# Kernel optimization log

Hardware: AMD Instinct MI355X
Metric: run time of the kernel (lower is better)

## Reference

```python
import jax, jax.numpy as jnp
import numpy as np
from jax import lax

LAYER_NUM = 6
EPS = 1e-9
BN_EPS = 1e-5

# CNOT ring on 3 qubits: CNOT(0,1), CNOT(1,2), CNOT(2,0); qubit 0 = MSB.
_P = np.zeros((8, 8), np.float32)
for _b in range(8):
    b0, b1, b2 = (_b >> 2) & 1, (_b >> 1) & 1, _b & 1
    b1 ^= b0
    b2 ^= b1
    b0 ^= b2
    _P[(b0 << 2) | (b1 << 1) | b2, _b] = 1.0
CNOT_RING = jnp.asarray(_P)


def _ry(t):
    c, s = jnp.cos(t / 2), jnp.sin(t / 2)
    return jnp.stack([jnp.stack([c, -s]), jnp.stack([s, c])])


def _channel_unitary(wc):
    # wc: [layer_num, 3] rotation angles -> full 8x8 circuit unitary (real, RY+CNOT)
    U = jnp.eye(8, dtype=wc.dtype)
    for l in range(wc.shape[0]):
        K = jnp.kron(jnp.kron(_ry(wc[l, 0]), _ry(wc[l, 1])), _ry(wc[l, 2]))
        U = CNOT_RING @ K @ U
    return U


def qcnn(x, weights, out_dim, out_size):
    # x: [B, C, H, W]; weights: [C, layer_num, 3]; 2x2 kernel, stride 2, no padding
    B, C, H, W = x.shape
    OH, OW = H // 2, W // 2
    # im2col: [B, C*4, OH, OW] with feature dim ordered (C, kh, kw)
    patches = lax.conv_general_dilated_patches(x, (2, 2), (2, 2), 'VALID')
    patches = patches.reshape(B, C, 4, OH * OW).transpose(0, 1, 3, 2)  # [B,C,P,4]
    # amplitude embedding on 2 data qubits, ancilla (MSB) in |0>
    nrm = jnp.linalg.norm(patches, axis=-1, keepdims=True)
    amp = patches / jnp.maximum(nrm, EPS)
    psi0 = jnp.pad(amp, ((0, 0), (0, 0), (0, 0), (0, 4)))  # [B,C,P,8]
    U = jax.vmap(_channel_unitary)(weights)  # [C,8,8]
    psi = jnp.einsum('cjk,bcpk->bcpj', U, psi0)
    probs = psi * psi
    data = probs[..., :4]  # post-select ancilla = 0
    data = data / jnp.maximum(data.sum(-1, keepdims=True), EPS)
    return data.reshape(B, out_dim, out_size, out_size)


def batchnorm2d(x, gamma, beta):
    mean = x.mean(axis=(0, 2, 3), keepdims=True)
    var = x.var(axis=(0, 2, 3), keepdims=True)
    xn = (x - mean) * lax.rsqrt(var + BN_EPS)
    return xn * gamma[None, :, None, None] + beta[None, :, None, None]


def setup_inputs() -> dict:
    key = jax.random.key(0)
    ks = jax.random.split(key, 5)
    return {
        'z': jax.random.normal(ks[0], (1024, 256, 4, 4), jnp.float32),
        'w1': jax.random.normal(ks[1], (256, LAYER_NUM, 3), jnp.float32),
        'w2': jax.random.normal(ks[2], (64, LAYER_NUM, 3), jnp.float32),
        'w3': jax.random.normal(ks[3], (16, LAYER_NUM, 3), jnp.float32),
        'w4': jax.random.normal(ks[4], (4, LAYER_NUM, 3), jnp.float32),
        'gamma2': jnp.ones((64,), jnp.float32), 'beta2': jnp.zeros((64,), jnp.float32),
        'gamma3': jnp.ones((16,), jnp.float32), 'beta3': jnp.zeros((16,), jnp.float32),
        'gamma4': jnp.ones((4,), jnp.float32), 'beta4': jnp.zeros((4,), jnp.float32),
        'gamma_f': jnp.ones((1,), jnp.float32), 'beta_f': jnp.zeros((1,), jnp.float32),
    }


def reference(z, w1, w2, w3, w4, gamma2, beta2, gamma3, beta3, gamma4, beta4, gamma_f, beta_f):
    s1 = qcnn(z, w1, 64, 8)
    x = jax.nn.relu(batchnorm2d(s1, gamma2, beta2))
    s2 = qcnn(x, w2, 16, 16)
    x = jax.nn.relu(batchnorm2d(s2, gamma3, beta3))
    s3 = qcnn(x, w3, 4, 32)
    x = jax.nn.relu(batchnorm2d(s3, gamma4, beta4))
    s4 = qcnn(x, w4, 1, 64)
    s4_bn = batchnorm2d(s4, gamma_f, beta_f)
    return jnp.tanh(s4_bn), s4, s4_bn
```

## Files before the change

kernel.cpp:

```cpp
#include <hip/hip_runtime.h>
#include <math.h>


#define NB 1024

__global__ __launch_bounds__(256) void build_V_kernel(
    const float* __restrict__ w1, const float* __restrict__ w2,
    const float* __restrict__ w3, const float* __restrict__ w4,
    float* __restrict__ V, float* __restrict__ acc)
{
    int t = blockIdx.x * blockDim.x + threadIdx.x;
    int j = t - 512;
    if (j >= 0 && j < 1360) acc[j] = 0.0f;
    if (t >= 340) return;
    const float* w; float* vout;
    if (t < 256)      { w = w1 + t*18;        vout = V + t*16; }
    else if (t < 320) { w = w2 + (t-256)*18;  vout = V + 4096 + (t-256)*16; }
    else if (t < 336) { w = w3 + (t-320)*18;  vout = V + 5120 + (t-320)*16; }
    else              { w = w4 + (t-336)*18;  vout = V + 5376 + (t-336)*16; }
    const int perm[8] = {0,5,7,2,3,6,4,1};
    float U[8][8];
    #pragma unroll
    for (int i=0;i<8;i++)
        #pragma unroll
        for (int jj=0;jj<8;jj++) U[i][jj] = (i==jj) ? 1.0f : 0.0f;
    for (int l=0;l<6;l++){
        float c0 = cosf(0.5f*w[l*3+0]), s0 = sinf(0.5f*w[l*3+0]);
        float c1 = cosf(0.5f*w[l*3+1]), s1 = sinf(0.5f*w[l*3+1]);
        float c2 = cosf(0.5f*w[l*3+2]), s2 = sinf(0.5f*w[l*3+2]);
        #pragma unroll
        for (int col=0; col<8; col++){
            float v[8];
            #pragma unroll
            for (int r=0;r<8;r++) v[r] = U[r][col];
            #pragma unroll
            for (int bb=0;bb<8;bb+=2){ float x=v[bb], y=v[bb+1]; v[bb]=c2*x-s2*y; v[bb+1]=s2*x+c2*y; }
            #pragma unroll
            for (int g=0;g<8;g+=4)
                #pragma unroll
                for (int i=0;i<2;i++){ int a=g+i, bq=g+i+2; float x=v[a], y=v[bq]; v[a]=c1*x-s1*y; v[bq]=s1*x+c1*y; }
            #pragma unroll
            for (int i=0;i<4;i++){ float x=v[i], y=v[i+4]; v[i]=c0*x-s0*y; v[i+4]=s0*x+c0*y; }
            #pragma unroll
            for (int r=0;r<8;r++) U[perm[r]][col] = v[r];
        }
    }
    #pragma unroll
    for (int jj=0;jj<4;jj++)
        #pragma unroll
        for (int k=0;k<4;k++) vout[jj*4+k] = U[jj][k];
}

template<int C, int H, int W, bool BN>
__global__ __launch_bounds__(256) void qcnn_kernel(
    const float* __restrict__ x, const float* __restrict__ V,
    const float* __restrict__ accPrev, const float* __restrict__ gamma,
    const float* __restrict__ beta, float invN,
    float* __restrict__ out, float* __restrict__ accOut)
{
    constexpr int HW  = H*W;
    constexpr int P   = HW/4;
    constexpr int OW  = W/2;
    constexpr int LP  = (P==4)?2:(P==16)?4:(P==64)?6:8;
    constexpr int LOW = (OW==2)?1:(OW==4)?2:(OW==8)?3:4;
    constexpr int OC  = C/4;
    constexpr int OCB = (64/P) < 1 ? 1 : (64/P);
    constexpr int G   = (4*P < 64) ? 4*P : 64;

    __shared__ float sBin[2*OCB];
    __shared__ float sSc[C], sSh[C];
    const int tid = threadIdx.x;

    if (tid < 2*OCB) sBin[tid] = 0.0f;
    if constexpr (BN){
        if (tid < C){
            float s=0.0f, q=0.0f;
            #pragma unroll
            for (int bk=0;bk<8;bk++){
                s += accPrev[bk*2*C + tid];
                q += accPrev[bk*2*C + C + tid];
            }
            float mean = s*invN;
            float var  = q*invN - mean*mean;
            float r    = 1.0f / sqrtf(var + 1e-5f);
            float sc   = gamma[tid]*r;
            sSc[tid] = sc;
            sSh[tid] = beta[tid] - mean*sc;
        }
    }
    __syncthreads();

    const int r0  = (blockIdx.x & 3) * 256;
    const int oc0 = r0 >> (LP+2);

    for (int it=0; it<4; ++it){
        int tg = (it<<18) + (blockIdx.x<<8) + tid;
        int b  = tg >> 10;
        int r  = tg & 1023;
        int c  = r >> LP;
        int p  = r & (P-1);
        int oh = p >> LOW;
        int ow = p & (OW-1);
        const float* xb = x + ((size_t)b<<12) + c*HW + (oh*2)*W + (ow*2);
        float2 t0 = *reinterpret_cast<const float2*>(xb);
        float2 t1 = *reinterpret_cast<const float2*>(xb + W);
        float x0=t0.x, x1=t0.y, x2=t1.x, x3=t1.y;
        if constexpr (BN){
            float sc = sSc[c], sh = sSh[c];
            x0 = fmaxf(fmaf(x0,sc,sh), 0.0f);
            x1 = fmaxf(fmaf(x1,sc,sh), 0.0f);
            x2 = fmaxf(fmaf(x2,sc,sh), 0.0f);
            x3 = fmaxf(fmaf(x3,sc,sh), 0.0f);
        }
        float nrm = sqrtf(x0*x0 + x1*x1 + x2*x2 + x3*x3);
        float inv = 1.0f / fmaxf(nrm, 1e-9f);
        float a0=x0*inv, a1=x1*inv, a2=x2*inv, a3=x3*inv;
        const float4* Vc = reinterpret_cast<const float4*>(V + (c<<4));
        float4 v0 = Vc[0], v1 = Vc[1], v2 = Vc[2], v3 = Vc[3];
        float q0 = v0.x*a0 + v0.y*a1 + v0.z*a2 + v0.w*a3;
        float q1 = v1.x*a0 + v1.y*a1 + v1.z*a2 + v1.w*a3;
        float q2 = v2.x*a0 + v2.y*a1 + v2.z*a2 + v2.w*a3;
        float q3 = v3.x*a0 + v3.y*a1 + v3.z*a2 + v3.w*a3;
        q0*=q0; q1*=q1; q2*=q2; q3*=q3;
        float dinv = 1.0f / fmaxf(q0+q1+q2+q3, 1e-9f);
        float d0=q0*dinv, d1=q1*dinv, d2=q2*dinv, d3=q3*dinv;
        *reinterpret_cast<float4*>(out + ((size_t)b<<12) + (r<<2)) =
            make_float4(d0,d1,d2,d3);
        float ls  = d0+d1+d2+d3;
        float lss = d0*d0 + d1*d1 + d2*d2 + d3*d3;
        #pragma unroll
        for (int off=1; off<G; off<<=1){
            ls  += __shfl_xor(ls,  off);
            lss += __shfl_xor(lss, off);
        }
        if ((tid & (G-1)) == 0){
            int ocl = (r >> (LP+2)) - oc0;
            atomicAdd(&sBin[ocl], ls);
            atomicAdd(&sBin[OCB + ocl], lss);
        }
    }
    __syncthreads();
    if (tid < OCB){
        int bank = blockIdx.x & 7;
        atomicAdd(&accOut[bank*2*OC + oc0 + tid],      sBin[tid]);
        atomicAdd(&accOut[bank*2*OC + OC + oc0 + tid], sBin[OCB + tid]);
    }
}

__global__ __launch_bounds__(256) void final_kernel(
    const float* __restrict__ s4, const float* __restrict__ acc4,
    const float* __restrict__ gf, const float* __restrict__ bf,
    float* __restrict__ out_tanh, float* __restrict__ out_bn)
{
    __shared__ float sP[2];
    if (threadIdx.x == 0){
        float s=0.0f, q=0.0f;
        #pragma unroll
        for (int bk=0;bk<8;bk++){ s += acc4[bk*2]; q += acc4[bk*2+1]; }
        float mean = s*(1.0f/4194304.0f);
        float var  = q*(1.0f/4194304.0f) - mean*mean;
        float r    = 1.0f / sqrtf(var + 1e-5f);
        float sc   = gf[0]*r;
        sP[0] = sc;
        sP[1] = bf[0] - mean*sc;
    }
    __syncthreads();
    float sc = sP[0], sh = sP[1];
    int i = blockIdx.x*blockDim.x + threadIdx.x;
    float4 v = reinterpret_cast<const float4*>(s4)[i];
    float4 bn = make_float4(fmaf(v.x,sc,sh), fmaf(v.y,sc,sh),
                            fmaf(v.z,sc,sh), fmaf(v.w,sc,sh));
    reinterpret_cast<float4*>(out_bn)[i] = bn;
    reinterpret_cast<float4*>(out_tanh)[i] =
        make_float4(tanhf(bn.x), tanhf(bn.y), tanhf(bn.z), tanhf(bn.w));
}

extern "C" void kernel_launch(void* const* d_in, const int* in_sizes, int n_in,
                              void* d_out, int out_size, void* d_ws, size_t ws_size,
                              hipStream_t stream)
{
    const float* z      = (const float*)d_in[0];
    const float* w1     = (const float*)d_in[1];
    const float* w2     = (const float*)d_in[2];
    const float* w3     = (const float*)d_in[3];
    const float* w4     = (const float*)d_in[4];
    const float* gamma2 = (const float*)d_in[5];
    const float* beta2  = (const float*)d_in[6];
    const float* gamma3 = (const float*)d_in[7];
    const float* beta3  = (const float*)d_in[8];
    const float* gamma4 = (const float*)d_in[9];
    const float* beta4  = (const float*)d_in[10];
    const float* gammaf = (const float*)d_in[11];
    const float* betaf  = (const float*)d_in[12];
    float* out = (float*)d_out;
    float* ws  = (float*)d_ws;

    float* V    = ws;
    float* acc  = ws + 8192;
    float* acc1 = acc;
    float* acc2 = acc + 1024;
    float* acc3 = acc + 1280;
    float* acc4 = acc + 1344;
    float* bufA = ws + 16384;
    float* bufB = ws + 16384 + 4194304;

    float* out_tanh = out;
    float* s4       = out + 4194304;
    float* out_bn   = out + 8388608;

    build_V_kernel<<<8, 256, 0, stream>>>(w1, w2, w3, w4, V, acc);

    qcnn_kernel<256,4,4,false><<<NB, 256, 0, stream>>>(
        z, V, nullptr, nullptr, nullptr, 0.0f, bufA, acc1);
    qcnn_kernel<64,8,8,true><<<NB, 256, 0, stream>>>(
        bufA, V+4096, acc1, gamma2, beta2, 1.0f/65536.0f, bufB, acc2);
    qcnn_kernel<16,16,16,true><<<NB, 256, 0, stream>>>(
        bufB, V+5120, acc2, gamma3, beta3, 1.0f/262144.0f, bufA, acc3);
    qcnn_kernel<4,32,32,true><<<NB, 256, 0, stream>>>(
        bufA, V+5376, acc3, gamma4, beta4, 1.0f/1048576.0f, s4, acc4);
    final_kernel<<<4096, 256, 0, stream>>>(
        s4, acc4, gammaf, betaf, out_tanh, out_bn);
}
```

Baseline: 176.0 us.

## Recompute QCNN stages from input per pass instead of storing intermediates

Replaces the four per-layer kernels that wrote and reread full intermediate tensors with a per-batch fused pass kernel. Each thread holds 64 values in registers and recomputes all earlier layers from z, emitting only per-batch partial BN statistics. A small stats kernel then reduces those partials into scale and shift, replacing the global atomics. This trades extra recomputation and repeated reads of z for removing the intermediate buffer traffic. It also swaps tanhf for an exp-based fast tanh, which may change precision slightly.

```diff
diff --git a/kernel.cpp b/kernel.cpp
--- a/kernel.cpp
+++ b/kernel.cpp
@@ -1,17 +1,13 @@
 #include <hip/hip_runtime.h>
 #include <math.h>
 
-
-#define NB 1024
 
 __global__ __launch_bounds__(256) void build_V_kernel(
     const float* __restrict__ w1, const float* __restrict__ w2,
     const float* __restrict__ w3, const float* __restrict__ w4,
-    float* __restrict__ V, float* __restrict__ acc)
+    float* __restrict__ V)
 {
     int t = blockIdx.x * blockDim.x + threadIdx.x;
-    int j = t - 512;
-    if (j >= 0 && j < 1360) acc[j] = 0.0f;
     if (t >= 340) return;
     const float* w; float* vout;
     if (t < 256)      { w = w1 + t*18;        vout = V + t*16; }
@@ -51,128 +47,234 @@
         for (int k=0;k<4;k++) vout[jj*4+k] = U[jj][k];
 }
 
-template<int C, int H, int W, bool BN>
-__global__ __launch_bounds__(256) void qcnn_kernel(
-    const float* __restrict__ x, const float* __restrict__ V,
-    const float* __restrict__ accPrev, const float* __restrict__ gamma,
-    const float* __restrict__ beta, float invN,
-    float* __restrict__ out, float* __restrict__ accOut)
-{
-    constexpr int HW  = H*W;
-    constexpr int P   = HW/4;
-    constexpr int OW  = W/2;
-    constexpr int LP  = (P==4)?2:(P==16)?4:(P==64)?6:8;
-    constexpr int LOW = (OW==2)?1:(OW==4)?2:(OW==8)?3:4;
-    constexpr int OC  = C/4;
-    constexpr int OCB = (64/P) < 1 ? 1 : (64/P);
-    constexpr int G   = (4*P < 64) ? 4*P : 64;
-
-    __shared__ float sBin[2*OCB];
-    __shared__ float sSc[C], sSh[C];
-    const int tid = threadIdx.x;
-
-    if (tid < 2*OCB) sBin[tid] = 0.0f;
-    if constexpr (BN){
-        if (tid < C){
+__device__ __forceinline__ void qstep(
+    float x0, float x1, float x2, float x3,
+    float4 v0, float4 v1, float4 v2, float4 v3, float* o)
+{
+    float nrm = sqrtf(x0*x0 + x1*x1 + x2*x2 + x3*x3);
+    float inv = 1.0f / fmaxf(nrm, 1e-9f);
+    float a0=x0*inv, a1=x1*inv, a2=x2*inv, a3=x3*inv;
+    float q0 = v0.x*a0 + v0.y*a1 + v0.z*a2 + v0.w*a3;
+    float q1 = v1.x*a0 + v1.y*a1 + v1.z*a2 + v1.w*a3;
+    float q2 = v2.x*a0 + v2.y*a1 + v2.z*a2 + v2.w*a3;
+    float q3 = v3.x*a0 + v3.y*a1 + v3.z*a2 + v3.w*a3;
+    q0*=q0; q1*=q1; q2*=q2; q3*=q3;
+    float dinv = 1.0f / fmaxf(q0+q1+q2+q3, 1e-9f);
+    o[0]=q0*dinv; o[1]=q1*dinv; o[2]=q2*dinv; o[3]=q3*dinv;
+}
+
+template<int NL, bool WS4>
+__global__ __launch_bounds__(128) void pass_kernel(
+    const float* __restrict__ z, const float* __restrict__ V,
+    const float* __restrict__ sc2, const float* __restrict__ sh2,
+    const float* __restrict__ sc3, const float* __restrict__ sh3,
+    const float* __restrict__ sc4, const float* __restrict__ sh4,
+    float* __restrict__ part, float* __restrict__ s4out)
+{
+    __shared__ __align__(16) float4 lds[2048];
+    const int tid   = threadIdx.x;
+    const int batch = blockIdx.x*2 + (tid>>6);
+    const int L     = tid & 63;
+
+    const float4* z4 = reinterpret_cast<const float4*>(z) + (size_t)blockIdx.x*2048;
+    #pragma unroll
+    for (int k=0;k<16;k++){
+        int G = k*128 + tid;
+        lds[(G & ~15) | ((G & 15) ^ ((G >> 4) & 7))] = z4[G];
+    }
+    __syncthreads();
+
+    float d[64];
+    #pragma unroll
+    for (int f=0; f<16; f++){
+        float4 v = lds[tid*16 + (f ^ (tid & 7))];
+        d[4*f+0]=v.x; d[4*f+1]=v.y; d[4*f+2]=v.z; d[4*f+3]=v.w;
+    }
+
+    #pragma unroll
+    for (int j=0;j<4;j++){
+        const float4* Vc = reinterpret_cast<const float4*>(V) + (size_t)(L*4+j)*4;
+        float4 v0=Vc[0], v1=Vc[1], v2=Vc[2], v3=Vc[3];
+        float t[16];
+        #pragma unroll
+        for (int p=0;p<4;p++){
+            int oh=p>>1, ow=p&1;
+            int base = j*16 + oh*8 + ow*2;
+            qstep(d[base], d[base+1], d[base+4], d[base+5], v0,v1,v2,v3, &t[p*4]);
+        }
+        #pragma unroll
+        for (int i=0;i<16;i++) d[j*16+i] = t[i];
+    }
+    if constexpr (NL==1){
+        float s=0.0f, q=0.0f;
+        #pragma unroll
+        for (int i=0;i<64;i++){ s += d[i]; q += d[i]*d[i]; }
+        part[batch*128 + L*2    ] = s;
+        part[batch*128 + L*2 + 1] = q;
+        return;
+    }
+
+    if constexpr (NL>=2){
+        { float sc = sc2[L], sh = sh2[L];
+          #pragma unroll
+          for (int i=0;i<64;i++) d[i] = fmaxf(fmaf(d[i],sc,sh), 0.0f); }
+        {
+            const float4* Vc = reinterpret_cast<const float4*>(V + 4096) + (size_t)L*4;
+            float4 v0=Vc[0], v1=Vc[1], v2=Vc[2], v3=Vc[3];
+            #pragma unroll
+            for (int oh=0;oh<4;oh++){
+                float t[16];
+                #pragma unroll
+                for (int ow=0;ow<4;ow++){
+                    int base = oh*16 + ow*2;
+                    qstep(d[base], d[base+1], d[base+8], d[base+9], v0,v1,v2,v3, &t[ow*4]);
+                }
+                #pragma unroll
+                for (int i=0;i<16;i++) d[oh*16+i] = t[i];
+            }
+        }
+        if constexpr (NL==2){
             float s=0.0f, q=0.0f;
             #pragma unroll
-            for (int bk=0;bk<8;bk++){
-                s += accPrev[bk*2*C + tid];
-                q += accPrev[bk*2*C + C + tid];
-            }
-            float mean = s*invN;
-            float var  = q*invN - mean*mean;
-            float r    = 1.0f / sqrtf(var + 1e-5f);
-            float sc   = gamma[tid]*r;
-            sSc[tid] = sc;
-            sSh[tid] = beta[tid] - mean*sc;
-        }
-    }
+            for (int i=0;i<64;i++){ s += d[i]; q += d[i]*d[i]; }
+            s += __shfl_xor(s,1); q += __shfl_xor(q,1);
+            s += __shfl_xor(s,2); q += __shfl_xor(q,2);
+            if ((L&3)==0){
+                int oc = L>>2;
+                part[batch*32 + oc*2    ] = s;
+                part[batch*32 + oc*2 + 1] = q;
+            }
+            return;
+        }
+    }
+
+    if constexpr (NL>=3){
+        { float sc = sc3[L>>2], sh = sh3[L>>2];
+          #pragma unroll
+          for (int i=0;i<64;i++) d[i] = fmaxf(fmaf(d[i],sc,sh), 0.0f); }
+        {
+            const int c3 = L>>2;
+            const float4* Vc = reinterpret_cast<const float4*>(V + 5120) + (size_t)c3*4;
+            float4 v0=Vc[0], v1=Vc[1], v2=Vc[2], v3=Vc[3];
+            #pragma unroll
+            for (int s5=0;s5<2;s5++){
+                float t[32];
+                #pragma unroll
+                for (int ow=0;ow<8;ow++){
+                    int base = s5*32 + ow*2;
+                    qstep(d[base], d[base+1], d[base+16], d[base+17], v0,v1,v2,v3, &t[ow*4]);
+                }
+                #pragma unroll
+                for (int i=0;i<32;i++) d[s5*32+i] = t[i];
+            }
+        }
+        if constexpr (NL==3){
+            float s=0.0f, q=0.0f;
+            #pragma unroll
+            for (int i=0;i<64;i++){ s += d[i]; q += d[i]*d[i]; }
+            #pragma unroll
+            for (int off=1; off<16; off<<=1){ s += __shfl_xor(s,off); q += __shfl_xor(q,off); }
+            if ((L&15)==0){
+                int oc = L>>4;
+                part[batch*8 + oc*2    ] = s;
+                part[batch*8 + oc*2 + 1] = q;
+            }
+            return;
+        }
+    }
+
+    if constexpr (NL>=4){
+        { float sc = sc4[L>>4], sh = sh4[L>>4];
+          #pragma unroll
+          for (int i=0;i<64;i++) d[i] = fmaxf(fmaf(d[i],sc,sh), 0.0f); }
+        {
+            const int c4 = L>>4;
+            const float4* Vc = reinterpret_cast<const float4*>(V + 5376) + (size_t)c4*4;
+            float4 v0=Vc[0], v1=Vc[1], v2=Vc[2], v3=Vc[3];
+            float t[32];
+            #pragma unroll
+            for (int i=0;i<32;i++) t[i] = d[32+i];
+            #pragma unroll
+            for (int ow=15; ow>=0; ow--){
+                qstep(d[2*ow], d[2*ow+1], t[2*ow], t[2*ow+1], v0,v1,v2,v3, &d[4*ow]);
+            }
+        }
+        {
+            float s=0.0f, q=0.0f;
+            #pragma unroll
+            for (int i=0;i<64;i++){ s += d[i]; q += d[i]*d[i]; }
+            #pragma unroll
+            for (int off=1; off<64; off<<=1){ s += __shfl_xor(s,off); q += __shfl_xor(q,off); }
+            if (L==0){
+                part[batch*2    ] = s;
+                part[batch*2 + 1] = q;
+            }
+        }
+        if constexpr (WS4){
+            __syncthreads();
+            #pragma unroll
+            for (int f=0;f<16;f++)
+                lds[tid*16 + (f ^ (tid & 7))] =
+                    make_float4(d[4*f], d[4*f+1], d[4*f+2], d[4*f+3]);
+            __syncthreads();
+            float4* o4 = reinterpret_cast<float4*>(s4out) + (size_t)blockIdx.x*2048;
+            #pragma unroll
+            for (int k=0;k<16;k++){
+                int G = k*128 + tid;
+                o4[G] = lds[(G & ~15) | ((G & 15) ^ ((G >> 4) & 7))];
+            }
+        }
+    }
+}
+
+__global__ __launch_bounds__(256) void stats_kernel(
+    const float* __restrict__ part, int OC,
+    const float* __restrict__ gamma, const float* __restrict__ beta,
+    float invN, float* __restrict__ scale, float* __restrict__ shift)
+{
+    __shared__ float sh8[8];
+    int oc = blockIdx.x;
+    float s=0.0f, q=0.0f;
+    for (int b=threadIdx.x; b<1024; b+=256){
+        s += part[b*2*OC + oc*2    ];
+        q += part[b*2*OC + oc*2 + 1];
+    }
+    #pragma unroll
+    for (int off=32; off; off>>=1){ s += __shfl_down(s,off); q += __shfl_down(q,off); }
+    int wid = threadIdx.x >> 6, lane = threadIdx.x & 63;
+    if (lane==0){ sh8[wid]=s; sh8[4+wid]=q; }
     __syncthreads();
-
-    const int r0  = (blockIdx.x & 3) * 256;
-    const int oc0 = r0 >> (LP+2);
-
-    for (int it=0; it<4; ++it){
-        int tg = (it<<18) + (blockIdx.x<<8) + tid;
-        int b  = tg >> 10;
-        int r  = tg & 1023;
-        int c  = r >> LP;
-        int p  = r & (P-1);
-        int oh = p >> LOW;
-        int ow = p & (OW-1);
-        const float* xb = x + ((size_t)b<<12) + c*HW + (oh*2)*W + (ow*2);
-        float2 t0 = *reinterpret_cast<const float2*>(xb);
-        float2 t1 = *reinterpret_cast<const float2*>(xb + W);
-        float x0=t0.x, x1=t0.y, x2=t1.x, x3=t1.y;
-        if constexpr (BN){
-            float sc = sSc[c], sh = sSh[c];
-            x0 = fmaxf(fmaf(x0,sc,sh), 0.0f);
-            x1 = fmaxf(fmaf(x1,sc,sh), 0.0f);
-            x2 = fmaxf(fmaf(x2,sc,sh), 0.0f);
-            x3 = fmaxf(fmaf(x3,sc,sh), 0.0f);
-        }
-        float nrm = sqrtf(x0*x0 + x1*x1 + x2*x2 + x3*x3);
-        float inv = 1.0f / fmaxf(nrm, 1e-9f);
-        float a0=x0*inv, a1=x1*inv, a2=x2*inv, a3=x3*inv;
-        const float4* Vc = reinterpret_cast<const float4*>(V + (c<<4));
-        float4 v0 = Vc[0], v1 = Vc[1], v2 = Vc[2], v3 = Vc[3];
-        float q0 = v0.x*a0 + v0.y*a1 + v0.z*a2 + v0.w*a3;
-        float q1 = v1.x*a0 + v1.y*a1 + v1.z*a2 + v1.w*a3;
-        float q2 = v2.x*a0 + v2.y*a1 + v2.z*a2 + v2.w*a3;
-        float q3 = v3.x*a0 + v3.y*a1 + v3.z*a2 + v3.w*a3;
-        q0*=q0; q1*=q1; q2*=q2; q3*=q3;
-        float dinv = 1.0f / fmaxf(q0+q1+q2+q3, 1e-9f);
-        float d0=q0*dinv, d1=q1*dinv, d2=q2*dinv, d3=q3*dinv;
-        *reinterpret_cast<float4*>(out + ((size_t)b<<12) + (r<<2)) =
-            make_float4(d0,d1,d2,d3);
-        float ls  = d0+d1+d2+d3;
-        float lss = d0*d0 + d1*d1 + d2*d2 + d3*d3;
-        #pragma unroll
-        for (int off=1; off<G; off<<=1){
-            ls  += __shfl_xor(ls,  off);
-            lss += __shfl_xor(lss, off);
-        }
-        if ((tid & (G-1)) == 0){
-            int ocl = (r >> (LP+2)) - oc0;
-            atomicAdd(&sBin[ocl], ls);
-            atomicAdd(&sBin[OCB + ocl], lss);
-        }
-    }
-    __syncthreads();
-    if (tid < OCB){
-        int bank = blockIdx.x & 7;
-        atomicAdd(&accOut[bank*2*OC + oc0 + tid],      sBin[tid]);
-        atomicAdd(&accOut[bank*2*OC + OC + oc0 + tid], sBin[OCB + tid]);
-    }
+    if (threadIdx.x==0){
+        s = sh8[0]+sh8[1]+sh8[2]+sh8[3];
+        q = sh8[4]+sh8[5]+sh8[6]+sh8[7];
+        float mean = s*invN;
+        float var  = q*invN - mean*mean;
+        float r    = 1.0f / sqrtf(var + 1e-5f);
+        float sc   = gamma[oc]*r;
+        scale[oc] = sc;
+        shift[oc] = beta[oc] - mean*sc;
+    }
+}
+
+__device__ __forceinline__ float fast_tanh(float x){
+    float e = __expf(2.0f*x);
+    return 1.0f - 2.0f/(e + 1.0f);
 }
 
 __global__ __launch_bounds__(256) void final_kernel(
-    const float* __restrict__ s4, const float* __restrict__ acc4,
-    const float* __restrict__ gf, const float* __restrict__ bf,
-    float* __restrict__ out_tanh, float* __restrict__ out_bn)
-{
-    __shared__ float sP[2];
-    if (threadIdx.x == 0){
-        float s=0.0f, q=0.0f;
-        #pragma unroll
-        for (int bk=0;bk<8;bk++){ s += acc4[bk*2]; q += acc4[bk*2+1]; }
-        float mean = s*(1.0f/4194304.0f);
-        float var  = q*(1.0f/4194304.0f) - mean*mean;
-        float r    = 1.0f / sqrtf(var + 1e-5f);
-        float sc   = gf[0]*r;
-        sP[0] = sc;
-        sP[1] = bf[0] - mean*sc;
-    }
-    __syncthreads();
-    float sc = sP[0], sh = sP[1];
+    const float* __restrict__ s4, const float* __restrict__ scf,
+    const float* __restrict__ shf, float* __restrict__ out_tanh,
+    float* __restrict__ out_bn)
+{
+    float sc = scf[0], sh = shf[0];
     int i = blockIdx.x*blockDim.x + threadIdx.x;
     float4 v = reinterpret_cast<const float4*>(s4)[i];
     float4 bn = make_float4(fmaf(v.x,sc,sh), fmaf(v.y,sc,sh),
                             fmaf(v.z,sc,sh), fmaf(v.w,sc,sh));
     reinterpret_cast<float4*>(out_bn)[i] = bn;
     reinterpret_cast<float4*>(out_tanh)[i] =
-        make_float4(tanhf(bn.x), tanhf(bn.y), tanhf(bn.z), tanhf(bn.w));
+        make_float4(fast_tanh(bn.x), fast_tanh(bn.y),
+                    fast_tanh(bn.z), fast_tanh(bn.w));
 }
 
 extern "C" void kernel_launch(void* const* d_in, const int* in_sizes, int n_in,
@@ -195,29 +297,41 @@
     float* out = (float*)d_out;
     float* ws  = (float*)d_ws;
 
-    float* V    = ws;
-    float* acc  = ws + 8192;
-    float* acc1 = acc;
-    float* acc2 = acc + 1024;
-    float* acc3 = acc + 1280;
-    float* acc4 = acc + 1344;
-    float* bufA = ws + 16384;
-    float* bufB = ws + 16384 + 4194304;
+    float* V     = ws;
+    float* sc2   = ws + 6144;  float* sh2 = ws + 6208;
+    float* sc3   = ws + 6272;  float* sh3 = ws + 6336;
+    float* sc4   = ws + 6400;  float* sh4 = ws + 6464;
+    float* scf   = ws + 6528;  float* shf = ws + 6592;
+    float* part1 = ws + 8192;
+    float* part2 = part1 + 131072;
+    float* part3 = part2 + 32768;
+    float* part4 = part3 + 8192;
 
     float* out_tanh = out;
     float* s4       = out + 4194304;
     float* out_bn   = out + 8388608;
 
-    build_V_kernel<<<8, 256, 0, stream>>>(w1, w2, w3, w4, V, acc);
-
-    qcnn_kernel<256,4,4,false><<<NB, 256, 0, stream>>>(
-        z, V, nullptr, nullptr, nullptr, 0.0f, bufA, acc1);
-    qcnn_kernel<64,8,8,true><<<NB, 256, 0, stream>>>(
-        bufA, V+4096, acc1, gamma2, beta2, 1.0f/65536.0f, bufB, acc2);
-    qcnn_kernel<16,16,16,true><<<NB, 256, 0, stream>>>(
-        bufB, V+5120, acc2, gamma3, beta3, 1.0f/262144.0f, bufA, acc3);
-    qcnn_kernel<4,32,32,true><<<NB, 256, 0, stream>>>(
-        bufA, V+5376, acc3, gamma4, beta4, 1.0f/1048576.0f, s4, acc4);
-    final_kernel<<<4096, 256, 0, stream>>>(
-        s4, acc4, gammaf, betaf, out_tanh, out_bn);
-}
+    build_V_kernel<<<2, 256, 0, stream>>>(w1, w2, w3, w4, V);
+
+    pass_kernel<1,false><<<512, 128, 0, stream>>>(
+        z, V, nullptr,nullptr, nullptr,nullptr, nullptr,nullptr, part1, nullptr);
+    stats_kernel<<<64, 256, 0, stream>>>(part1, 64, gamma2, beta2,
+        1.0f/65536.0f, sc2, sh2);
+
+    pass_kernel<2,false><<<512, 128, 0, stream>>>(
+        z, V, sc2,sh2, nullptr,nullptr, nullptr,nullptr, part2, nullptr);
+    stats_kernel<<<16, 256, 0, stream>>>(part2, 16, gamma3, beta3,
+        1.0f/262144.0f, sc3, sh3);
+
+    pass_kernel<3,false><<<512, 128, 0, stream>>>(
+        z, V, sc2,sh2, sc3,sh3, nullptr,nullptr, part3, nullptr);
+    stats_kernel<<<4, 256, 0, stream>>>(part3, 4, gamma4, beta4,
+        1.0f/1048576.0f, sc4, sh4);
+
+    pass_kernel<4,true><<<512, 128, 0, stream>>>(
+        z, V, sc2,sh2, sc3,sh3, sc4,sh4, part4, s4);
+    stats_kernel<<<1, 256, 0, stream>>>(part4, 1, gammaf, betaf,
+        1.0f/4194304.0f, scf, shf);
+
+    final_kernel<<<4096, 256, 0, stream>>>(s4, scf, shf, out_tanh, out_bn);
+}
```

Result: slower. 183.8 us (+4.4%).

## Finalize batchnorm stats in last-arriving block and use fast tanh

Applied to the files above, without the earlier changes.

Replaces global float atomics into banked accumulators with per-block partial-sum slots, plus a completion counter. The last block to finish reduces the partials and writes per-channel scale and shift, so consumer kernels no longer recompute the BN parameters in every block. The final kernel now uses an exp-based tanh approximation. The last-block pattern adds a threadfence and a global atomic per block, and the fast tanh may lose precision or overflow handling for large inputs.

```diff
diff --git a/kernel.cpp b/kernel.cpp
--- a/kernel.cpp
+++ b/kernel.cpp
@@ -7,11 +7,10 @@
 __global__ __launch_bounds__(256) void build_V_kernel(
     const float* __restrict__ w1, const float* __restrict__ w2,
     const float* __restrict__ w3, const float* __restrict__ w4,
-    float* __restrict__ V, float* __restrict__ acc)
+    float* __restrict__ V, int* __restrict__ cnts)
 {
     int t = blockIdx.x * blockDim.x + threadIdx.x;
-    int j = t - 512;
-    if (j >= 0 && j < 1360) acc[j] = 0.0f;
+    if (t < 4) cnts[t] = 0;
     if (t >= 340) return;
     const float* w; float* vout;
     if (t < 256)      { w = w1 + t*18;        vout = V + t*16; }
@@ -54,9 +53,11 @@
 template<int C, int H, int W, bool BN>
 __global__ __launch_bounds__(256) void qcnn_kernel(
     const float* __restrict__ x, const float* __restrict__ V,
-    const float* __restrict__ accPrev, const float* __restrict__ gamma,
-    const float* __restrict__ beta, float invN,
-    float* __restrict__ out, float* __restrict__ accOut)
+    const float* __restrict__ scPrev, const float* __restrict__ shPrev,
+    float* __restrict__ out, float* __restrict__ psum, float* __restrict__ pssq,
+    const float* __restrict__ gammaN, const float* __restrict__ betaN,
+    float invN, float* __restrict__ scaleN, float* __restrict__ shiftN,
+    int* __restrict__ cnt)
 {
     constexpr int HW  = H*W;
     constexpr int P   = HW/4;
@@ -66,28 +67,14 @@
     constexpr int OC  = C/4;
     constexpr int OCB = (64/P) < 1 ? 1 : (64/P);
     constexpr int G   = (4*P < 64) ? 4*P : 64;
+    constexpr int DIV   = OC/OCB < 1 ? 1 : OC/OCB;
+    constexpr int NSLOT = NB/DIV;
+    constexpr int TPO   = (256/OC < 64) ? 256/OC : 64;
 
     __shared__ float sBin[2*OCB];
-    __shared__ float sSc[C], sSh[C];
+    __shared__ int lastFlag;
     const int tid = threadIdx.x;
-
     if (tid < 2*OCB) sBin[tid] = 0.0f;
-    if constexpr (BN){
-        if (tid < C){
-            float s=0.0f, q=0.0f;
-            #pragma unroll
-            for (int bk=0;bk<8;bk++){
-                s += accPrev[bk*2*C + tid];
-                q += accPrev[bk*2*C + C + tid];
-            }
-            float mean = s*invN;
-            float var  = q*invN - mean*mean;
-            float r    = 1.0f / sqrtf(var + 1e-5f);
-            float sc   = gamma[tid]*r;
-            sSc[tid] = sc;
-            sSh[tid] = beta[tid] - mean*sc;
-        }
-    }
     __syncthreads();
 
     const int r0  = (blockIdx.x & 3) * 256;
@@ -106,7 +93,7 @@
         float2 t1 = *reinterpret_cast<const float2*>(xb + W);
         float x0=t0.x, x1=t0.y, x2=t1.x, x3=t1.y;
         if constexpr (BN){
-            float sc = sSc[c], sh = sSh[c];
+            float sc = scPrev[c], sh = shPrev[c];
             x0 = fmaxf(fmaf(x0,sc,sh), 0.0f);
             x1 = fmaxf(fmaf(x1,sc,sh), 0.0f);
             x2 = fmaxf(fmaf(x2,sc,sh), 0.0f);
@@ -141,38 +128,59 @@
     }
     __syncthreads();
     if (tid < OCB){
-        int bank = blockIdx.x & 7;
-        atomicAdd(&accOut[bank*2*OC + oc0 + tid],      sBin[tid]);
-        atomicAdd(&accOut[bank*2*OC + OC + oc0 + tid], sBin[OCB + tid]);
-    }
+        int slot = blockIdx.x / DIV;
+        psum[(oc0 + tid)*NSLOT + slot] = sBin[tid];
+        pssq[(oc0 + tid)*NSLOT + slot] = sBin[OCB + tid];
+    }
+    __threadfence();
+    __syncthreads();
+    if (tid == 0) lastFlag = (atomicAdd(cnt, 1) == NB-1) ? 1 : 0;
+    __syncthreads();
+    if (lastFlag){
+        __threadfence();
+        int oc = tid / TPO;
+        if (oc < OC){
+            float s=0.0f, q=0.0f;
+            for (int s0 = tid % TPO; s0 < NSLOT; s0 += TPO){
+                s += psum[oc*NSLOT + s0];
+                q += pssq[oc*NSLOT + s0];
+            }
+            #pragma unroll
+            for (int off=1; off<TPO; off<<=1){
+                s += __shfl_xor(s, off);
+                q += __shfl_xor(q, off);
+            }
+            if ((tid % TPO) == 0){
+                float mean = s*invN;
+                float var  = q*invN - mean*mean;
+                float r    = 1.0f / sqrtf(var + 1e-5f);
+                float sc   = gammaN[oc]*r;
+                scaleN[oc] = sc;
+                shiftN[oc] = betaN[oc] - mean*sc;
+            }
+        }
+    }
+}
+
+__device__ __forceinline__ float fast_tanh(float x){
+    float e = __expf(2.0f*x);
+    return 1.0f - 2.0f/(e + 1.0f);
 }
 
 __global__ __launch_bounds__(256) void final_kernel(
-    const float* __restrict__ s4, const float* __restrict__ acc4,
-    const float* __restrict__ gf, const float* __restrict__ bf,
-    float* __restrict__ out_tanh, float* __restrict__ out_bn)
-{
-    __shared__ float sP[2];
-    if (threadIdx.x == 0){
-        float s=0.0f, q=0.0f;
-        #pragma unroll
-        for (int bk=0;bk<8;bk++){ s += acc4[bk*2]; q += acc4[bk*2+1]; }
-        float mean = s*(1.0f/4194304.0f);
-        float var  = q*(1.0f/4194304.0f) - mean*mean;
-        float r    = 1.0f / sqrtf(var + 1e-5f);
-        float sc   = gf[0]*r;
-        sP[0] = sc;
-        sP[1] = bf[0] - mean*sc;
-    }
-    __syncthreads();
-    float sc = sP[0], sh = sP[1];
+    const float* __restrict__ s4, const float* __restrict__ scf,
+    const float* __restrict__ shf, float* __restrict__ out_tanh,
+    float* __restrict__ out_bn)
+{
+    float sc = scf[0], sh = shf[0];
     int i = blockIdx.x*blockDim.x + threadIdx.x;
     float4 v = reinterpret_cast<const float4*>(s4)[i];
     float4 bn = make_float4(fmaf(v.x,sc,sh), fmaf(v.y,sc,sh),
                             fmaf(v.z,sc,sh), fmaf(v.w,sc,sh));
     reinterpret_cast<float4*>(out_bn)[i] = bn;
     reinterpret_cast<float4*>(out_tanh)[i] =
-        make_float4(tanhf(bn.x), tanhf(bn.y), tanhf(bn.z), tanhf(bn.w));
+        make_float4(fast_tanh(bn.x), fast_tanh(bn.y),
+                    fast_tanh(bn.z), fast_tanh(bn.w));
 }
 
 extern "C" void kernel_launch(void* const* d_in, const int* in_sizes, int n_in,
@@ -196,28 +204,36 @@
     float* ws  = (float*)d_ws;
 
     float* V    = ws;
-    float* acc  = ws + 8192;
-    float* acc1 = acc;
-    float* acc2 = acc + 1024;
-    float* acc3 = acc + 1280;
-    float* acc4 = acc + 1344;
-    float* bufA = ws + 16384;
-    float* bufB = ws + 16384 + 4194304;
+    float* sc2  = ws + 6144;  float* sh2 = ws + 6208;
+    float* sc3  = ws + 6272;  float* sh3 = ws + 6336;
+    float* sc4  = ws + 6400;  float* sh4 = ws + 6464;
+    float* scf  = ws + 6528;  float* shf = ws + 6592;
+    int*   cnts = (int*)(ws + 6656);
+    float* p1s  = ws + 8192;   float* p1q = ws + 24576;
+    float* p2s  = ws + 40960;  float* p2q = ws + 45056;
+    float* p3s  = ws + 49152;  float* p3q = ws + 50176;
+    float* p4s  = ws + 51200;  float* p4q = ws + 52224;
+    float* bufA = ws + 65536;
+    float* bufB = ws + 65536 + 4194304;
 
     float* out_tanh = out;
     float* s4       = out + 4194304;
     float* out_bn   = out + 8388608;
 
-    build_V_kernel<<<8, 256, 0, stream>>>(w1, w2, w3, w4, V, acc);
+    build_V_kernel<<<2, 256, 0, stream>>>(w1, w2, w3, w4, V, cnts);
 
     qcnn_kernel<256,4,4,false><<<NB, 256, 0, stream>>>(
-        z, V, nullptr, nullptr, nullptr, 0.0f, bufA, acc1);
+        z, V, nullptr, nullptr, bufA, p1s, p1q,
+        gamma2, beta2, 1.0f/65536.0f, sc2, sh2, cnts+0);
     qcnn_kernel<64,8,8,true><<<NB, 256, 0, stream>>>(
-        bufA, V+4096, acc1, gamma2, beta2, 1.0f/65536.0f, bufB, acc2);
+        bufA, V+4096, sc2, sh2, bufB, p2s, p2q,
+        gamma3, beta3, 1.0f/262144.0f, sc3, sh3, cnts+1);
     qcnn_kernel<16,16,16,true><<<NB, 256, 0, stream>>>(
-        bufB, V+5120, acc2, gamma3, beta3, 1.0f/262144.0f, bufA, acc3);
+        bufB, V+5120, sc3, sh3, bufA, p3s, p3q,
+        gamma4, beta4, 1.0f/1048576.0f, sc4, sh4, cnts+2);
     qcnn_kernel<4,32,32,true><<<NB, 256, 0, stream>>>(
-        bufA, V+5376, acc3, gamma4, beta4, 1.0f/1048576.0f, s4, acc4);
-    final_kernel<<<4096, 256, 0, stream>>>(
-        s4, acc4, gammaf, betaf, out_tanh, out_bn);
-}
+        bufA, V+5376, sc4, sh4, s4, p4s, p4q,
+        gammaf, betaf, 1.0f/4194304.0f, scf, shf, cnts+3);
+
+    final_kernel<<<4096, 256, 0, stream>>>(s4, scf, shf, out_tanh, out_bn);
+}
```

After: 510.6 us. 190% more time.
